# Kernel tuning notes

Measured on AMD Instinct MI355X. Metric: run time of the kernel, lower is better.

## Reference

```python
import jax, jax.numpy as jnp
import numpy as np

WS = 8
NUM_HEADS = 8
BLUR_STRENGTH = 1.0
EPS = 1e-5


def setup_inputs() -> dict:
    key = jax.random.key(0)
    ks = jax.random.split(key, 8)
    B, C, H, W = 8, 256, 128, 128
    FF = 1024
    inp = {
        'x': jax.random.normal(ks[0], (B, C, H, W), jnp.float32),
        'blur_map': jax.random.uniform(ks[1], (B, 1, H // 4, W // 4), jnp.float32),
        'qkv_w': jax.random.normal(ks[2], (C, 3 * C), jnp.float32) * 0.02,
        'qkv_b': jnp.zeros((3 * C,), jnp.float32),
        'proj_w': jax.random.normal(ks[3], (C, C), jnp.float32) * 0.02,
        'proj_b': jnp.zeros((C,), jnp.float32),
        'ff1_w': jax.random.normal(ks[4], (C, FF), jnp.float32) * 0.02,
        'ff1_b': jnp.zeros((FF,), jnp.float32),
        'ff2_w': jax.random.normal(ks[5], (FF, C), jnp.float32) * 0.02,
        'ff2_b': jnp.zeros((C,), jnp.float32),
        'n1_g': jnp.ones((C,), jnp.float32),
        'n1_b': jnp.zeros((C,), jnp.float32),
        'n2_g': jnp.ones((C,), jnp.float32),
        'n2_b': jnp.zeros((C,), jnp.float32),
    }
    return inp


def _layer_norm(y, g, b):
    mu = jnp.mean(y, axis=-1, keepdims=True)
    var = jnp.mean(jnp.square(y - mu), axis=-1, keepdims=True)
    return (y - mu) * jax.lax.rsqrt(var + EPS) * g + b


def reference(x, blur_map, qkv_w, qkv_b, proj_w, proj_b, ff1_w, ff1_b, ff2_w, ff2_b, n1_g, n1_b, n2_g, n2_b):
    B, C, H, W = x.shape
    ws = WS
    h = NUM_HEADS
    hd = C // h
    T = ws * ws
    scale = C ** (-0.5)  # note: full dim, matching the torch module

    # window partition -> [nw, T, C]
    xw = x.reshape(B, C, H // ws, ws, W // ws, ws)
    xw = xw.transpose(0, 2, 4, 3, 5, 1).reshape(-1, T, C)
    nw = xw.shape[0]

    qkv = (xw @ qkv_w + qkv_b).reshape(nw, T, 3, h, hd).transpose(2, 0, 3, 1, 4)
    q, k, v = qkv[0], qkv[1], qkv[2]  # [nw, h, T, hd]

    attn = jnp.einsum('whid,whjd->whij', q, k) * scale

    # blur modulation along the key axis
    blur_down = jax.image.resize(blur_map, (B, 1, H, W), 'bilinear')
    blur_w = blur_down.reshape(B, 1, H // ws, ws, W // ws, ws)
    blur_w = blur_w.transpose(0, 2, 4, 3, 5, 1).reshape(nw, T)
    attn = attn * (1.0 + BLUR_STRENGTH * blur_w)[:, None, None, :]

    attn = jax.nn.softmax(attn, axis=-1)
    out = jnp.einsum('whij,whjd->whid', attn, v)
    out = out.transpose(0, 2, 1, 3).reshape(nw, T, C)
    out = out @ proj_w + proj_b

    x1 = xw + _layer_norm(out, n1_g, n1_b)
    ff = jnp.maximum(x1 @ ff1_w + ff1_b, 0.0) @ ff2_w + ff2_b
    x2 = x1 + _layer_norm(ff, n2_g, n2_b)

    # window reverse -> [B, C, H, W]
    x2 = x2.reshape(B, H // ws, W // ws, ws, ws, C)
    return x2.transpose(0, 5, 1, 3, 2, 4).reshape(B, C, H, W)
```

## Files before the change

### kernel.cpp

```cpp
#include <hip/hip_runtime.h>
#include <hip/hip_bf16.h>
#include <cstdint>

typedef _Float16 half8 __attribute__((ext_vector_type(8)));
typedef _Float16 half4 __attribute__((ext_vector_type(4)));
typedef float f32x4 __attribute__((ext_vector_type(4)));

__device__ __forceinline__ void gload_lds16(const _Float16* g, _Float16* l) {
  __builtin_amdgcn_global_load_lds(
      (const __attribute__((address_space(1))) void*)g,
      (__attribute__((address_space(3))) void*)l, 16, 0, 0);
}

#define KSWZ(r) ((((r) >> 1) & 3) << 3)

__global__ __launch_bounds__(256) void wtrans_all(
    const float* __restrict__ qkv_w, const float* __restrict__ proj_w,
    const float* __restrict__ ff1_w, const float* __restrict__ ff2_w,
    _Float16* __restrict__ qwT, _Float16* __restrict__ pwT,
    _Float16* __restrict__ f1T, _Float16* __restrict__ f2T) {
  const int b = blockIdx.x;
  const float* W; _Float16* WT; int K, N, idx;
  if (b < 768)       { W = qkv_w;  WT = qwT; K = 256;  N = 768;  idx = b * 256 + threadIdx.x; }
  else if (b < 1024) { W = proj_w; WT = pwT; K = 256;  N = 256;  idx = (b - 768) * 256 + threadIdx.x; }
  else if (b < 2048) { W = ff1_w;  WT = f1T; K = 256;  N = 1024; idx = (b - 1024) * 256 + threadIdx.x; }
  else               { W = ff2_w;  WT = f2T; K = 1024; N = 256;  idx = (b - 2048) * 256 + threadIdx.x; }
  int k = idx / N, n = idx - k * N;
  WT[(size_t)n * K + k] = (_Float16)W[idx];
}

__global__ __launch_bounds__(256) void blur_prep(const float* __restrict__ bm,
                                                 float* __restrict__ bw) {
  int idx = blockIdx.x * 256 + threadIdx.x;
  int wi = idx >> 6, t = idx & 63;
  int b = wi >> 8, wid = wi & 255;
  int hw = wid >> 4, ww = wid & 15;
  int hh = hw * 8 + (t >> 3), www = ww * 8 + (t & 7);
  float yf = (hh + 0.5f) * 0.25f - 0.5f;
  float xf = (www + 0.5f) * 0.25f - 0.5f;
  float yfl = floorf(yf), xfl = floorf(xf);
  float fy = yf - yfl, fx = xf - xfl;
  int y0 = (int)yfl, x0 = (int)xfl;
  int y1 = y0 + 1, x1 = x0 + 1;
  if (y0 < 0) y0 = 0; if (x0 < 0) x0 = 0;
  if (y1 > 31) y1 = 31; if (x1 > 31) x1 = 31;
  const float* p = bm + (size_t)b * 1024;
  float v00 = p[y0 * 32 + x0], v01 = p[y0 * 32 + x1];
  float v10 = p[y1 * 32 + x0], v11 = p[y1 * 32 + x1];
  float v0 = v00 + fx * (v01 - v00);
  float v1 = v10 + fx * (v11 - v10);
  bw[idx] = v0 + fy * (v1 - v0);
}

__global__ __launch_bounds__(256) void gather_x(const float* __restrict__ x,
                                                _Float16* __restrict__ xw) {
  const int c0 = blockIdx.x << 6;
  const int hh = blockIdx.y;
  const int b  = blockIdx.z;
  __shared__ float tile[64][133];
  const int tid = threadIdx.x;
  {
    const int cl = tid >> 7, p = tid & 127;
    const float* xp = x + ((size_t)(b * 256 + c0) * 128 + hh) * 128 + p;
#pragma unroll
    for (int i = 0; i < 32; ++i) {
      int c = i * 2 + cl;
      tile[c][p] = xp[(size_t)c * 16384];
    }
  }
  __syncthreads();
  const int w = tid >> 6, lane = tid & 63;
  const int hw = hh >> 3, ts = hh & 7;
#pragma unroll
  for (int i = 0; i < 32; ++i) {
    int pp = i * 4 + w;
    int row = ((b * 256 + hw * 16 + (pp >> 3)) << 6) + ts * 8 + (pp & 7);
    xw[(size_t)row * 256 + c0 + lane] = (_Float16)tile[lane][pp];
  }
}

__global__ __launch_bounds__(256) void ln_scatter(const _Float16* __restrict__ rc,
    const _Float16* __restrict__ x1, const float* __restrict__ gg,
    const float* __restrict__ bb, float* __restrict__ out) {
  const int hh = blockIdx.x;
  const int b  = blockIdx.y;
  __shared__ _Float16 tile[128][258];
  const int w = threadIdx.x >> 6, lane = threadIdx.x & 63;
  const int hw = hh >> 3, ts = hh & 7;
  f32x4 gv = *(const f32x4*)(gg + lane * 4);
  f32x4 bv = *(const f32x4*)(bb + lane * 4);
#pragma unroll
  for (int i = 0; i < 32; ++i) {
    const int pp = w * 32 + i;
    const size_t row = ((size_t)(b * 256 + hw * 16 + (pp >> 3)) << 6) + ts * 8 + (pp & 7);
    half4 v  = ((const half4*)(rc + row * 256))[lane];
    half4 rv = ((const half4*)(x1 + row * 256))[lane];
    float f0 = (float)v[0], f1 = (float)v[1], f2 = (float)v[2], f3 = (float)v[3];
    float s = f0 + f1 + f2 + f3;
    float s2 = f0*f0 + f1*f1 + f2*f2 + f3*f3;
#pragma unroll
    for (int m = 1; m < 64; m <<= 1) {
      s  += __shfl_xor(s, m, 64);
      s2 += __shfl_xor(s2, m, 64);
    }
    float mu = s * 0.00390625f;
    float var = s2 * 0.00390625f - mu * mu;
    float rs = rsqrtf(var + 1e-5f);
    half4 ov;
    ov[0] = (_Float16)((f0 - mu) * rs * gv[0] + bv[0] + (float)rv[0]);
    ov[1] = (_Float16)((f1 - mu) * rs * gv[1] + bv[1] + (float)rv[1]);
    ov[2] = (_Float16)((f2 - mu) * rs * gv[2] + bv[2] + (float)rv[2]);
    ov[3] = (_Float16)((f3 - mu) * rs * gv[3] + bv[3] + (float)rv[3]);
    *(half4*)&tile[pp][lane * 4] = ov;
  }
  __syncthreads();
  const int cl = threadIdx.x >> 7, p = threadIdx.x & 127;
  float* op = out + ((size_t)(b * 256) * 128 + hh) * 128 + p;
#pragma unroll
  for (int i = 0; i < 128; ++i) {
    int c = i * 2 + cl;
    op[(size_t)c * 16384] = (float)tile[p][c];
  }
}

template<int RELU>
__global__ __launch_bounds__(512) void gemm_f16(const _Float16* __restrict__ A,
    const _Float16* __restrict__ BT, const float* __restrict__ bias,
    _Float16* __restrict__ C, int M, int N, int K) {
  __shared__ _Float16 As[3][128 * 32];
  __shared__ _Float16 Bs[3][128 * 32];
  const int tid = threadIdx.x;
  const int gx = gridDim.x;
  int flat = blockIdx.y * gx + blockIdx.x;
  int nwg = gx * gridDim.y;
  int nb = (nwg & 7) ? flat : ((flat & 7) * (nwg >> 3) + (flat >> 3));
  const int m0 = (nb / gx) << 7;
  const int n0 = (nb % gx) << 7;
  const int w = tid >> 6, lane = tid & 63;
  const int wr = (w >> 2) << 6;
  const int wc = (w & 3) << 5;
  const int lr = lane & 15, lg = lane >> 4;
  f32x4 acc[4][2] = {};
  const int sr = tid >> 2;
  const int skk = ((tid & 3) << 3) ^ KSWZ(tid >> 2);
  const _Float16* Ag = A + (size_t)(m0 + sr) * K + skk;
  const _Float16* Bg = BT + (size_t)(n0 + sr) * K + skk;
#define GSTAGE(bufi, k0) do { \
    gload_lds16(Ag + (k0), &As[bufi][(size_t)tid * 8]); \
    gload_lds16(Bg + (k0), &Bs[bufi][(size_t)tid * 8]); \
  } while (0)
  const int nsteps = K >> 5;
  GSTAGE(0, 0);
  GSTAGE(1, 32);
  int cur = 0;
  for (int t = 0; t < nsteps; ++t) {
    if (t + 1 < nsteps) {
      asm volatile("s_waitcnt vmcnt(2)" ::: "memory");
    } else {
      asm volatile("s_waitcnt vmcnt(0)" ::: "memory");
    }
    __builtin_amdgcn_s_barrier();
    half8 af[4], bf[2];
#pragma unroll
    for (int tt = 0; tt < 4; ++tt) {
      int rowA = wr + tt * 16 + lr;
      af[tt] = *(const half8*)&As[cur][rowA * 32 + ((lg * 8) ^ KSWZ(rowA))];
    }
#pragma unroll
    for (int tt = 0; tt < 2; ++tt) {
      int rowB = wc + tt * 16 + lr;
      bf[tt] = *(const half8*)&Bs[cur][rowB * 32 + ((lg * 8) ^ KSWZ(rowB))];
    }
#pragma unroll
    for (int i = 0; i < 4; ++i)
#pragma unroll
      for (int j = 0; j < 2; ++j)
        acc[i][j] = __builtin_amdgcn_mfma_f32_16x16x32_f16(af[i], bf[j], acc[i][j], 0, 0, 0);
    if (t + 2 < nsteps) {
      int nxt = cur + 2; if (nxt >= 3) nxt -= 3;
      GSTAGE(nxt, (t + 2) * 32);
    }
    cur = (cur == 2) ? 0 : cur + 1;
  }
#undef GSTAGE
  float bv[2];
#pragma unroll
  for (int j = 0; j < 2; ++j) bv[j] = bias[n0 + wc + j * 16 + lr];
#pragma unroll
  for (int i = 0; i < 4; ++i) {
#pragma unroll
    for (int j = 0; j < 2; ++j) {
      int row = m0 + wr + i * 16 + lg * 4;
      int col = n0 + wc + j * 16 + lr;
      _Float16* cp = C + (size_t)row * N + col;
#pragma unroll
      for (int rr = 0; rr < 4; ++rr) {
        float v = acc[i][j][rr] + bv[j];
        if (RELU) v = fmaxf(v, 0.0f);
        cp[(size_t)rr * N] = (_Float16)v;
      }
    }
  }
}

#define ATT_SWZ(row, col) (((row) << 6) + ((col) ^ (((row) & 7) << 3)))
__global__ __launch_bounds__(256, 3) void attn_mfma(const _Float16* __restrict__ qkv,
    const float* __restrict__ bw, _Float16* __restrict__ o) {
  const int wdw = blockIdx.x;
  const int w = threadIdx.x >> 6;
  const int lane = threadIdx.x & 63;
  const int lr = lane & 15, lg = lane >> 4;
  __shared__ _Float16 lds_p[4][64 * 64];
  __shared__ _Float16 lds_v[4][32 * 64];
  _Float16* Pb = lds_p[w];
  _Float16* Vt = lds_v[w];
  const size_t base = (size_t)wdw * 49152;
  f32x4 blv[4];
#pragma unroll
  for (int jt = 0; jt < 4; ++jt) {
    f32x4 bv = *(const f32x4*)&bw[wdw * 64 + jt * 16 + lg * 4];
    blv[jt] = bv * 0.0625f + 0.0625f;
  }
  const f32x4 zero4 = {0.f, 0.f, 0.f, 0.f};
#pragma unroll
  for (int hi = 0; hi < 2; ++hi) {
    const int h = w + hi * 4;
    const size_t qo = base + (size_t)h * 32;
    const _Float16* kp = qkv + qo + 256 + (size_t)lr * 768 + lg * 8;
    const _Float16* qp = qkv + qo +       (size_t)lr * 768 + lg * 8;
    half8 ak[4], bq[4];
#pragma unroll
    for (int t = 0; t < 4; ++t) {
      ak[t] = *(const half8*)(kp + (size_t)t * 16 * 768);
      bq[t] = *(const half8*)(qp + (size_t)t * 16 * 768);
    }
    const _Float16* vp = qkv + qo + 512 + (size_t)lane * 768;
#pragma unroll
    for (int e = 0; e < 4; ++e) {
      half8 vv = *(const half8*)(vp + e * 8);
#pragma unroll
      for (int d = 0; d < 8; ++d) Vt[ATT_SWZ(e * 8 + d, lane)] = vv[d];
    }
    f32x4 cst[4][4];
    __builtin_amdgcn_s_setprio(1);
#pragma unroll
    for (int jt = 0; jt < 4; ++jt)
#pragma unroll
      for (int it = 0; it < 4; ++it)
        cst[jt][it] = __builtin_amdgcn_mfma_f32_16x16x32_f16(ak[jt], bq[it], zero4, 0, 0, 0);
    __builtin_amdgcn_s_setprio(0);
#pragma unroll
    for (int it = 0; it < 4; ++it) {
      float m = -1e30f;
#pragma unroll
      for (int jt = 0; jt < 4; ++jt) {
        cst[jt][it] *= blv[jt];
        m = fmaxf(m, fmaxf(fmaxf(cst[jt][it][0], cst[jt][it][1]),
                           fmaxf(cst[jt][it][2], cst[jt][it][3])));
      }
      m = fmaxf(m, __shfl_xor(m, 16, 64));
      m = fmaxf(m, __shfl_xor(m, 32, 64));
      float s = 0.f;
#pragma unroll
      for (int jt = 0; jt < 4; ++jt)
#pragma unroll
        for (int r = 0; r < 4; ++r) {
          float e = __expf(cst[jt][it][r] - m);
          cst[jt][it][r] = e;
          s += e;
        }
      s += __shfl_xor(s, 16, 64);
      s += __shfl_xor(s, 32, 64);
      float inv = 1.0f / s;
#pragma unroll
      for (int jt = 0; jt < 4; ++jt) {
        half4 pv;
#pragma unroll
        for (int r = 0; r < 4; ++r) pv[r] = (_Float16)(cst[jt][it][r] * inv);
        *(half4*)&Pb[ATT_SWZ(it * 16 + lr, jt * 16 + lg * 4)] = pv;
      }
    }
    f32x4 co[4][2] = {};
#pragma unroll
    for (int ks = 0; ks < 2; ++ks) {
      half8 bv2[2], pa[4];
#pragma unroll
      for (int dt = 0; dt < 2; ++dt)
        bv2[dt] = *(const half8*)&Vt[ATT_SWZ(dt * 16 + lr, ks * 32 + lg * 8)];
#pragma unroll
      for (int it = 0; it < 4; ++it)
        pa[it] = *(const half8*)&Pb[ATT_SWZ(it * 16 + lr, ks * 32 + lg * 8)];
      __builtin_amdgcn_s_setprio(1);
#pragma unroll
      for (int it = 0; it < 4; ++it)
#pragma unroll
        for (int dt = 0; dt < 2; ++dt)
          co[it][dt] = __builtin_amdgcn_mfma_f32_16x16x32_f16(pa[it], bv2[dt], co[it][dt], 0, 0, 0);
      __builtin_amdgcn_s_setprio(0);
    }
#pragma unroll
    for (int it = 0; it < 4; ++it)
#pragma unroll
      for (int dt = 0; dt < 2; ++dt)
#pragma unroll
        for (int r = 0; r < 4; ++r) {
          int row = it * 16 + lg * 4 + r;
          o[((size_t)wdw * 64 + row) * 256 + h * 32 + dt * 16 + lr] =
              (_Float16)co[it][dt][r];
        }
  }
}

__global__ __launch_bounds__(256) void ln_add(const _Float16* __restrict__ inp,
    const _Float16* __restrict__ res, const float* __restrict__ gg,
    const float* __restrict__ bb, _Float16* __restrict__ out) {
  const int w = threadIdx.x >> 6, lane = threadIdx.x & 63;
  const size_t row = (size_t)blockIdx.x * 4 + w;
  half4 v = ((const half4*)(inp + row * 256))[lane];
  float f0 = (float)v[0], f1 = (float)v[1], f2 = (float)v[2], f3 = (float)v[3];
  float s = f0 + f1 + f2 + f3;
  float s2 = f0*f0 + f1*f1 + f2*f2 + f3*f3;
#pragma unroll
  for (int m = 1; m < 64; m <<= 1) {
    s  += __shfl_xor(s, m, 64);
    s2 += __shfl_xor(s2, m, 64);
  }
  float mu = s * 0.00390625f;
  float var = s2 * 0.00390625f - mu * mu;
  float rs = rsqrtf(var + 1e-5f);
  f32x4 gv = *(const f32x4*)(gg + lane * 4);
  f32x4 bv = *(const f32x4*)(bb + lane * 4);
  half4 rv = ((const half4*)(res + row * 256))[lane];
  half4 ov;
  ov[0] = (_Float16)((f0 - mu) * rs * gv[0] + bv[0] + (float)rv[0]);
  ov[1] = (_Float16)((f1 - mu) * rs * gv[1] + bv[1] + (float)rv[1]);
  ov[2] = (_Float16)((f2 - mu) * rs * gv[2] + bv[2] + (float)rv[2]);
  ov[3] = (_Float16)((f3 - mu) * rs * gv[3] + bv[3] + (float)rv[3]);
  ((half4*)(out + row * 256))[lane] = ov;
}

__global__ __launch_bounds__(256) void sentinel(float* out, int n) {
  int i = blockIdx.x * 256 + threadIdx.x;
  if (i < n) out[i] = 12345.0f;
}

extern "C" void kernel_launch(void* const* d_in, const int* in_sizes, int n_in,
                              void* d_out, int out_size, void* d_ws, size_t ws_size,
                              hipStream_t stream) {
  const float* x      = (const float*)d_in[0];
  const float* blurm  = (const float*)d_in[1];
  const float* qkv_w  = (const float*)d_in[2];
  const float* qkv_b  = (const float*)d_in[3];
  const float* proj_w = (const float*)d_in[4];
  const float* proj_b = (const float*)d_in[5];
  const float* ff1_w  = (const float*)d_in[6];
  const float* ff1_b  = (const float*)d_in[7];
  const float* ff2_w  = (const float*)d_in[8];
  const float* ff2_b  = (const float*)d_in[9];
  const float* n1_g   = (const float*)d_in[10];
  const float* n1_b   = (const float*)d_in[11];
  const float* n2_g   = (const float*)d_in[12];
  const float* n2_b   = (const float*)d_in[13];
  float* out = (float*)d_out;

  char* ws = (char*)d_ws;
  constexpr size_t OFF_RA  = 0;
  constexpr size_t OFF_XW  = 201326592ull;
  constexpr size_t OFF_AO  = OFF_XW + 67108864ull;
  constexpr size_t OFF_RC  = OFF_AO + 67108864ull;
  constexpr size_t OFF_X1  = OFF_RC + 67108864ull;
  constexpr size_t OFF_QW  = OFF_X1 + 67108864ull;
  constexpr size_t OFF_PW  = OFF_QW + 393216ull;
  constexpr size_t OFF_F1W = OFF_PW + 131072ull;
  constexpr size_t OFF_F2W = OFF_F1W + 524288ull;
  constexpr size_t OFF_BL  = OFF_F2W + 524288ull;
  constexpr size_t NEED    = OFF_BL + 524288ull;
  if (ws_size < NEED) {
    sentinel<<<(out_size + 255) / 256, 256, 0, stream>>>(out, out_size);
    return;
  }
  _Float16* RA   = (_Float16*)(ws + OFF_RA);
  _Float16* xw_h = (_Float16*)(ws + OFF_XW);
  _Float16* ao   = (_Float16*)(ws + OFF_AO);
  _Float16* rc   = (_Float16*)(ws + OFF_RC);
  _Float16* x1h  = (_Float16*)(ws + OFF_X1);
  _Float16* qwT  = (_Float16*)(ws + OFF_QW);
  _Float16* pwT  = (_Float16*)(ws + OFF_PW);
  _Float16* f1wT = (_Float16*)(ws + OFF_F1W);
  _Float16* f2wT = (_Float16*)(ws + OFF_F2W);
  float* blurw   = (float*)(ws + OFF_BL);

  wtrans_all<<<3072, 256, 0, stream>>>(qkv_w, proj_w, ff1_w, ff2_w, qwT, pwT, f1wT, f2wT);
  blur_prep<<<512, 256, 0, stream>>>(blurm, blurw);
  gather_x<<<dim3(4, 128, 8), 256, 0, stream>>>(x, xw_h);

  gemm_f16<0><<<dim3(6, 1024), 512, 0, stream>>>(xw_h, qwT, qkv_b, RA, 131072, 768, 256);
  attn_mfma<<<2048, 256, 0, stream>>>(RA, blurw, ao);
  gemm_f16<0><<<dim3(2, 1024), 512, 0, stream>>>(ao, pwT, proj_b, rc, 131072, 256, 256);
  ln_add<<<32768, 256, 0, stream>>>(rc, xw_h, n1_g, n1_b, x1h);
  for (int ch = 0; ch < 2; ++ch) {
    const size_t off = (size_t)ch * 65536 * 256;
    gemm_f16<1><<<dim3(8, 512), 512, 0, stream>>>(x1h + off, f1wT, ff1_b,
                                                  RA, 65536, 1024, 256);
    gemm_f16<0><<<dim3(2, 512), 512, 0, stream>>>(RA, f2wT, ff2_b,
                                                  rc + off, 65536, 256, 1024);
  }
  ln_scatter<<<dim3(128, 8), 256, 0, stream>>>(rc, x1h, n2_g, n2_b, out);
}
```

Before: 585.5 us.

## Fuse projection GEMM with LayerNorm and residual add into one kernel

Replaces the proj GEMM plus a separate ln_add kernel with a single kernel. Each block computes a full 128x256 output row tile, so LayerNorm statistics are reduced within the block via shuffles and a small shared buffer, then the residual is added and the result written directly. This removes the write and re-read of the intermediate projection output and one launch. In exchange, each block holds more accumulators, there is less parallelism per row tile (1024 blocks), and the epilogue stores are scalar and strided rather than vectorized.

```diff
diff --git a/kernel.cpp b/kernel.cpp
--- a/kernel.cpp
+++ b/kernel.cpp
@@ -203,6 +203,121 @@
   }
 }
 
+__global__ __launch_bounds__(512) void gemm_ln512(const _Float16* __restrict__ A,
+    const _Float16* __restrict__ BT, const float* __restrict__ bias,
+    const _Float16* __restrict__ resid, const float* __restrict__ gg,
+    const float* __restrict__ bb, _Float16* __restrict__ outp, int M) {
+  constexpr int K = 256;
+  __shared__ _Float16 As[3][128 * 32];
+  __shared__ _Float16 Bs[3][256 * 32];
+  __shared__ float part[128][4][2];
+  const int tid = threadIdx.x;
+  int flat = blockIdx.x;
+  int nwg = gridDim.x;
+  int nb = (nwg & 7) ? flat : ((flat & 7) * (nwg >> 3) + (flat >> 3));
+  const int m0 = nb << 7;
+  const int w = tid >> 6, lane = tid & 63;
+  const int wr = (w >> 2) << 6;
+  const int wc = (w & 3) << 6;
+  const int lr = lane & 15, lg = lane >> 4;
+  f32x4 acc[4][4] = {};
+  const int sr = tid >> 2;
+  const int skk = ((tid & 3) << 3) ^ KSWZ(tid >> 2);
+  const _Float16* Ag = A + (size_t)(m0 + sr) * K + skk;
+  const _Float16* Bg = BT + (size_t)sr * K + skk;
+  const size_t bstep = (size_t)128 * K;
+#define GSTAGE(bufi, k0) do { \
+    gload_lds16(Ag + (k0),         &As[bufi][(size_t)tid * 8]); \
+    gload_lds16(Bg + (k0),         &Bs[bufi][(size_t)tid * 8]); \
+    gload_lds16(Bg + (k0) + bstep, &Bs[bufi][(size_t)(512 + tid) * 8]); \
+  } while (0)
+  const int nsteps = K >> 5;
+  GSTAGE(0, 0);
+  GSTAGE(1, 32);
+  int cur = 0;
+  for (int t = 0; t < nsteps; ++t) {
+    if (t + 1 < nsteps) {
+      asm volatile("s_waitcnt vmcnt(3)" ::: "memory");
+    } else {
+      asm volatile("s_waitcnt vmcnt(0)" ::: "memory");
+    }
+    __builtin_amdgcn_s_barrier();
+    half8 af[4], bf[4];
+#pragma unroll
+    for (int tt = 0; tt < 4; ++tt) {
+      int rowA = wr + tt * 16 + lr;
+      af[tt] = *(const half8*)&As[cur][rowA * 32 + ((lg * 8) ^ KSWZ(rowA))];
+    }
+#pragma unroll
+    for (int tt = 0; tt < 4; ++tt) {
+      int rowB = wc + tt * 16 + lr;
+      bf[tt] = *(const half8*)&Bs[cur][rowB * 32 + ((lg * 8) ^ KSWZ(rowB))];
+    }
+#pragma unroll
+    for (int i = 0; i < 4; ++i)
+#pragma unroll
+      for (int j = 0; j < 4; ++j)
+        acc[i][j] = __builtin_amdgcn_mfma_f32_16x16x32_f16(af[i], bf[j], acc[i][j], 0, 0, 0);
+    if (t + 2 < nsteps) {
+      int nxt = cur + 2; if (nxt >= 3) nxt -= 3;
+      GSTAGE(nxt, (t + 2) * 32);
+    }
+    cur = (cur == 2) ? 0 : cur + 1;
+  }
+#undef GSTAGE
+  float bv4[4], gv4[4], bb4[4];
+#pragma unroll
+  for (int j = 0; j < 4; ++j) {
+    int col = wc + j * 16 + lr;
+    bv4[j] = bias[col]; gv4[j] = gg[col]; bb4[j] = bb[col];
+  }
+#pragma unroll
+  for (int i = 0; i < 4; ++i)
+#pragma unroll
+    for (int j = 0; j < 4; ++j)
+      acc[i][j] += f32x4{bv4[j], bv4[j], bv4[j], bv4[j]};
+#pragma unroll
+  for (int i = 0; i < 4; ++i)
+#pragma unroll
+    for (int rr = 0; rr < 4; ++rr) {
+      float s = 0.f, s2 = 0.f;
+#pragma unroll
+      for (int j = 0; j < 4; ++j) {
+        float v = acc[i][j][rr];
+        s += v; s2 += v * v;
+      }
+#pragma unroll
+      for (int mk = 1; mk < 16; mk <<= 1) {
+        s  += __shfl_xor(s, mk, 64);
+        s2 += __shfl_xor(s2, mk, 64);
+      }
+      if (lr == 0) {
+        int rl = wr + i * 16 + lg * 4 + rr;
+        part[rl][w & 3][0] = s;
+        part[rl][w & 3][1] = s2;
+      }
+    }
+  __syncthreads();
+#pragma unroll
+  for (int i = 0; i < 4; ++i)
+#pragma unroll
+    for (int rr = 0; rr < 4; ++rr) {
+      int rl = wr + i * 16 + lg * 4 + rr;
+      float s  = part[rl][0][0] + part[rl][1][0] + part[rl][2][0] + part[rl][3][0];
+      float s2 = part[rl][0][1] + part[rl][1][1] + part[rl][2][1] + part[rl][3][1];
+      float mu = s * 0.00390625f;
+      float rs = rsqrtf(s2 * 0.00390625f - mu * mu + 1e-5f);
+      const size_t row = (size_t)(m0 + rl);
+#pragma unroll
+      for (int j = 0; j < 4; ++j) {
+        int col = wc + j * 16 + lr;
+        float v = (acc[i][j][rr] - mu) * rs * gv4[j] + bb4[j]
+                  + (float)resid[row * 256 + col];
+        outp[row * 256 + col] = (_Float16)v;
+      }
+    }
+}
+
 #define ATT_SWZ(row, col) (((row) << 6) + ((col) ^ (((row) & 7) << 3)))
 __global__ __launch_bounds__(256, 3) void attn_mfma(const _Float16* __restrict__ qkv,
     const float* __restrict__ bw, _Float16* __restrict__ o) {
@@ -309,34 +424,6 @@
               (_Float16)co[it][dt][r];
         }
   }
-}
-
-__global__ __launch_bounds__(256) void ln_add(const _Float16* __restrict__ inp,
-    const _Float16* __restrict__ res, const float* __restrict__ gg,
-    const float* __restrict__ bb, _Float16* __restrict__ out) {
-  const int w = threadIdx.x >> 6, lane = threadIdx.x & 63;
-  const size_t row = (size_t)blockIdx.x * 4 + w;
-  half4 v = ((const half4*)(inp + row * 256))[lane];
-  float f0 = (float)v[0], f1 = (float)v[1], f2 = (float)v[2], f3 = (float)v[3];
-  float s = f0 + f1 + f2 + f3;
-  float s2 = f0*f0 + f1*f1 + f2*f2 + f3*f3;
-#pragma unroll
-  for (int m = 1; m < 64; m <<= 1) {
-    s  += __shfl_xor(s, m, 64);
-    s2 += __shfl_xor(s2, m, 64);
-  }
-  float mu = s * 0.00390625f;
-  float var = s2 * 0.00390625f - mu * mu;
-  float rs = rsqrtf(var + 1e-5f);
-  f32x4 gv = *(const f32x4*)(gg + lane * 4);
-  f32x4 bv = *(const f32x4*)(bb + lane * 4);
-  half4 rv = ((const half4*)(res + row * 256))[lane];
-  half4 ov;
-  ov[0] = (_Float16)((f0 - mu) * rs * gv[0] + bv[0] + (float)rv[0]);
-  ov[1] = (_Float16)((f1 - mu) * rs * gv[1] + bv[1] + (float)rv[1]);
-  ov[2] = (_Float16)((f2 - mu) * rs * gv[2] + bv[2] + (float)rv[2]);
-  ov[3] = (_Float16)((f3 - mu) * rs * gv[3] + bv[3] + (float)rv[3]);
-  ((half4*)(out + row * 256))[lane] = ov;
 }
 
 __global__ __launch_bounds__(256) void sentinel(float* out, int n) {
@@ -396,8 +483,7 @@
 
   gemm_f16<0><<<dim3(6, 1024), 512, 0, stream>>>(xw_h, qwT, qkv_b, RA, 131072, 768, 256);
   attn_mfma<<<2048, 256, 0, stream>>>(RA, blurw, ao);
-  gemm_f16<0><<<dim3(2, 1024), 512, 0, stream>>>(ao, pwT, proj_b, rc, 131072, 256, 256);
-  ln_add<<<32768, 256, 0, stream>>>(rc, xw_h, n1_g, n1_b, x1h);
+  gemm_ln512<<<1024, 512, 0, stream>>>(ao, pwT, proj_b, xw_h, n1_g, n1_b, x1h, 131072);
   for (int ch = 0; ch < 2; ++ch) {
     const size_t off = (size_t)ch * 65536 * 256;
     gemm_f16<1><<<dim3(8, 512), 512, 0, stream>>>(x1h + off, f1wT, ff1_b,
```

Result: no change. 585.3 us (-0.0%).
